# Optimization experiments

Hardware: AMD Instinct MI355X
Metric: run time of the kernel (lower is better)

## Reference

```python
import jax, jax.numpy as jnp
import numpy as np

# dims: B batch, N seq, D model_dim, R lora rank, C codebooks, K codebook_input_channel, P kv pairs, M per-codebook output
B, N, D, R, C, K, P = 4, 2048, 1024, 8, 64, 16, 64
M = (D * R) // C  # 128


def setup_inputs() -> dict:
    key = jax.random.key(0)
    ks = jax.random.split(key, 7)
    x = jax.random.normal(ks[0], (B, N, D), dtype=jnp.float32)
    W_A = jax.random.normal(ks[1], (C, K, D), dtype=jnp.float32) * (D ** -0.5)
    emb_A = jax.random.uniform(ks[2], (C, P, K), dtype=jnp.float32, minval=-1.5, maxval=1.5)
    vals_A = jax.random.normal(ks[3], (C, P, M), dtype=jnp.float32)
    W_B = jax.random.normal(ks[4], (C, K, D), dtype=jnp.float32) * (D ** -0.5)
    emb_B = jax.random.uniform(ks[5], (C, P, K), dtype=jnp.float32, minval=-1.5, maxval=1.5)
    vals_B = jax.random.normal(ks[6], (C, P, M), dtype=jnp.float32)
    return {"x": x, "W_A": W_A, "emb_A": emb_A, "vals_A": vals_A,
            "W_B": W_B, "emb_B": emb_B, "vals_B": vals_B}


def _discrete_kv(x, W, emb, vals):
    # x: [B,N,D]; W: [C,K,D] (Linear weight per codebook); emb: [C,P,K]; vals: [C,P,M]
    proj = jnp.einsum('bnd,ckd->cbnk', x, W)  # per-codebook linear projection
    # squared euclidean distance to each key (argmin is same as cdist argmin)
    d2 = (jnp.sum(proj * proj, axis=-1, keepdims=True)
          - 2.0 * jnp.einsum('cbnk,cpk->cbnp', proj, emb)
          + jnp.sum(emb * emb, axis=-1)[:, None, None, :])  # [C,B,N,P]
    idx = jnp.argmin(d2, axis=-1)                      # [C,B,N]
    y = jax.vmap(lambda v, i: v[i])(vals, idx)          # [C,B,N,M]
    # concat over codebooks on last dim -> [B,N,C*M], then view as [B,N,R,D]
    return jnp.transpose(y, (1, 2, 0, 3)).reshape(x.shape[0], x.shape[1], R, D)


def reference(x, W_A, emb_A, vals_A, W_B, emb_B, vals_B):
    A = _discrete_kv(x, W_A, emb_A, vals_A)   # [B,N,R,D]
    Bm = _discrete_kv(x, W_B, emb_B, vals_B)  # [B,N,R,D]
    t = jnp.einsum('bnd,bnrd->bnr', x, A)
    return jnp.einsum('bnr,bnrd->bnd', t, Bm)
```

## Files before the change

### kernel.cpp

```cpp
#include <hip/hip_runtime.h>

#define NTOK   8192
#define DMODEL 1024
#define NC     64
#define NK     16
#define NP     64
#define NM     128
#define LCAP   (1 << 18)
#define MARGIN 2e-3f

typedef _Float16 f16x8  __attribute__((ext_vector_type(8)));
typedef float    f32x16 __attribute__((ext_vector_type(16)));

#define AS1 __attribute__((address_space(1)))
#define AS3 __attribute__((address_space(3)))

__device__ __forceinline__ void glds16(const void* g, void* l) {
    __builtin_amdgcn_global_load_lds((const AS1 void*)g, (AS3 void*)l, 16, 0, 0);
}

__global__ __launch_bounds__(256) void k_split(
    const float* __restrict__ x, const float* __restrict__ W_A, const float* __restrict__ W_B,
    short* __restrict__ xh, short* __restrict__ xl,
    short* __restrict__ whA, short* __restrict__ wlA,
    short* __restrict__ whB, short* __restrict__ wlB)
{
    const int t = blockIdx.x * 256 + threadIdx.x;
    const int NX = 128 * NTOK;
    const int NW = 128 * 1024;

    const float* src;
    short *dh, *dl;
    if (t < NX) {
        const int chunk = t >> 13, tok = t & 8191;
        src = x + (size_t)tok * DMODEL + chunk * 8;
        dh = xh + (size_t)t * 8;  dl = xl + (size_t)t * 8;
    } else if (t < NX + NW) {
        const int u = t - NX, chunk = u >> 10, ck = u & 1023;
        src = W_A + (size_t)ck * DMODEL + chunk * 8;
        dh = whA + (size_t)u * 8; dl = wlA + (size_t)u * 8;
    } else {
        const int u = t - NX - NW, chunk = u >> 10, ck = u & 1023;
        src = W_B + (size_t)ck * DMODEL + chunk * 8;
        dh = whB + (size_t)u * 8; dl = wlB + (size_t)u * 8;
    }

    const float4 a = *(const float4*)src;
    const float4 b = *(const float4*)(src + 4);
    const float v[8] = {a.x, a.y, a.z, a.w, b.x, b.y, b.z, b.w};
    unsigned h[8], l[8];
    #pragma unroll
    for (int j = 0; j < 8; ++j) {
        const _Float16 hf = (_Float16)v[j];
        const _Float16 lf = (_Float16)(v[j] - (float)hf);
        h[j] = (unsigned)__builtin_bit_cast(unsigned short, hf);
        l[j] = (unsigned)__builtin_bit_cast(unsigned short, lf);
    }
    *(int4*)dh = make_int4((int)(h[0] | (h[1] << 16)), (int)(h[2] | (h[3] << 16)),
                           (int)(h[4] | (h[5] << 16)), (int)(h[6] | (h[7] << 16)));
    *(int4*)dl = make_int4((int)(l[0] | (l[1] << 16)), (int)(l[2] | (l[3] << 16)),
                           (int)(l[4] | (l[5] << 16)), (int)(l[6] | (l[7] << 16)));
}

__global__ __launch_bounds__(512, 1) void k_mfma_argmin(
    const short* __restrict__ xh, const short* __restrict__ xl,
    const short* __restrict__ whA, const short* __restrict__ wlA,
    const short* __restrict__ whB, const short* __restrict__ wlB,
    const float* __restrict__ emb_A, const float* __restrict__ emb_B,
    int* __restrict__ idxbuf, int* __restrict__ list, int* __restrict__ cnt)
{
    __shared__ __align__(16) float smem[32768];
    short* ls = (short*)smem;
    float* projT = smem;
    float* embS  = smem + 16640;
    float* e2S   = smem + 24832;

    const int tid = threadIdx.x;
    const int bid = blockIdx.x;
    const int swz = (bid & 7) * 32 + (bid >> 3);
    const int tb  = swz >> 3;
    const int ot  = swz & 7;
    const int set = ot >> 2;
    const short* __restrict__ wh = set ? whB : whA;
    const short* __restrict__ wl = set ? wlB : wlA;
    const float* __restrict__ Ep = set ? emb_B : emb_A;
    const int ckbase = (ot & 3) * 256;

    const int lane = tid & 63;
    const int wid  = tid >> 6;
    const int wr   = wid >> 2;
    const int wc   = wid & 3;
    const int lr31 = lane & 31;
    const int lk2  = lane >> 5;

    f32x16 acc[4][2];
    #pragma unroll
    for (int m = 0; m < 4; ++m)
        #pragma unroll
        for (int n = 0; n < 2; ++n)
            #pragma unroll
            for (int r = 0; r < 16; ++r) acc[m][n][r] = 0.f;

    const size_t oA0 = ((size_t)(tid >> 8) * NTOK + tb * 256 + (tid & 255)) * 8;
    const size_t oA1 = ((size_t)((tid + 512) >> 8) * NTOK + tb * 256 + (tid & 255)) * 8;
    const size_t oB0 = ((size_t)(tid >> 8) * 1024 + ckbase + (tid & 255)) * 8;
    const size_t oB1 = ((size_t)((tid + 512) >> 8) * 1024 + ckbase + (tid & 255)) * 8;

    #define STAGE(buf, st)                                                   \
        do {                                                                 \
            const size_t sa_ = (size_t)(st) * (4 * NTOK * 8);                \
            const size_t sb_ = (size_t)(st) * (4 * 1024 * 8);                \
            short* lb_ = ls + (buf) * 32768 + tid * 8;                       \
            glds16(xh + oA0 + sa_, lb_);                                     \
            glds16(xh + oA1 + sa_, lb_ + 4096);                              \
            glds16(xl + oA0 + sa_, lb_ + 8192);                              \
            glds16(xl + oA1 + sa_, lb_ + 12288);                             \
            glds16(wh + oB0 + sb_, lb_ + 16384);                             \
            glds16(wh + oB1 + sb_, lb_ + 20480);                             \
            glds16(wl + oB0 + sb_, lb_ + 24576);                             \
            glds16(wl + oB1 + sb_, lb_ + 28672);                             \
        } while (0)

    STAGE(0, 0);
    for (int t = 0; t < 32; ++t) {
        const int cur = t & 1;
        if (t < 31) {
            STAGE(cur ^ 1, t + 1);
            asm volatile("s_waitcnt vmcnt(8)" ::: "memory");
        } else {
            asm volatile("s_waitcnt vmcnt(0)" ::: "memory");
        }
        __builtin_amdgcn_sched_barrier(0);
        __builtin_amdgcn_s_barrier();

        const short* pbuf = ls + cur * 32768;
        #pragma unroll
        for (int ks = 0; ks < 2; ++ks) {
            const int kc2 = ks * 2 + lk2;
            const short* pa = pbuf + (kc2 * 256 + wr * 128 + lr31) * 8;
            const short* pB = pbuf + 16384 + (kc2 * 256 + wc * 64 + lr31) * 8;
            f16x8 ah[4], al[4], bh[2], bl[2];
            #pragma unroll
            for (int m = 0; m < 4; ++m) {
                ah[m] = *(const f16x8*)(pa + m * 256);
                al[m] = *(const f16x8*)(pa + 8192 + m * 256);
            }
            #pragma unroll
            for (int n = 0; n < 2; ++n) {
                bh[n] = *(const f16x8*)(pB + n * 256);
                bl[n] = *(const f16x8*)(pB + 8192 + n * 256);
            }
            #pragma unroll
            for (int m = 0; m < 4; ++m)
                #pragma unroll
                for (int n = 0; n < 2; ++n) {
                    acc[m][n] = __builtin_amdgcn_mfma_f32_32x32x16_f16(ah[m], bh[n], acc[m][n], 0, 0, 0);
                    acc[m][n] = __builtin_amdgcn_mfma_f32_32x32x16_f16(ah[m], bl[n], acc[m][n], 0, 0, 0);
                    acc[m][n] = __builtin_amdgcn_mfma_f32_32x32x16_f16(al[m], bh[n], acc[m][n], 0, 0, 0);
                }
        }
        __builtin_amdgcn_s_barrier();
    }
    #undef STAGE

    #pragma unroll
    for (int ch = 0; ch < 2; ++ch) {
        __syncthreads();
        {
            const float4* eg = (const float4*)(Ep + (size_t)((ot & 3) * 16 + ch * 8) * NP * NK);
            float4* es = (float4*)embS;
            #pragma unroll
            for (int i = 0; i < 4; ++i) es[tid + 512 * i] = eg[tid + 512 * i];
        }
        __syncthreads();
        {
            const float* e = embS + tid * 16;
            float s = 0.f;
            #pragma unroll
            for (int k = 0; k < 16; ++k) s = fmaf(e[k], e[k], s);
            e2S[tid] = s;
        }
        #pragma unroll
        for (int c = 0; c < 4; ++c) {
            __syncthreads();
            if (wr == (c >> 1)) {
                #pragma unroll
                for (int mi = 0; mi < 2; ++mi) {
                    const int m = (c & 1) * 2 + mi;
                    #pragma unroll
                    for (int n = 0; n < 2; ++n) {
                        const int col = wc * 64 + n * 32 + lr31;
                        #pragma unroll
                        for (int r = 0; r < 16; ++r) {
                            const int trow = mi * 32 + (r & 3) + 8 * (r >> 2) + 4 * lk2;
                            projT[col * 65 + trow] = acc[m][n][r];
                        }
                    }
                }
            }
            __syncthreads();
            {
                const int lt = tid & 63, cbl = tid >> 6;
                float pr[16];
                #pragma unroll
                for (int k = 0; k < 16; ++k)
                    pr[k] = projT[((ch * 8 + cbl) * 16 + k) * 65 + lt];
                const float4* eb4 = (const float4*)(embS + cbl * 1024);
                const float* e2 = e2S + cbl * 64;
                float best = 1e30f, second = 1e30f;
                int bp = 0;
                for (int p = 0; p < 64; ++p) {
                    const float4 e0 = eb4[p * 4 + 0], e1 = eb4[p * 4 + 1];
                    const float4 e2v = eb4[p * 4 + 2], e3 = eb4[p * 4 + 3];
                    float s = 0.f;
                    s = fmaf(pr[0], e0.x, s);   s = fmaf(pr[1], e0.y, s);
                    s = fmaf(pr[2], e0.z, s);   s = fmaf(pr[3], e0.w, s);
                    s = fmaf(pr[4], e1.x, s);   s = fmaf(pr[5], e1.y, s);
                    s = fmaf(pr[6], e1.z, s);   s = fmaf(pr[7], e1.w, s);
                    s = fmaf(pr[8], e2v.x, s);  s = fmaf(pr[9], e2v.y, s);
                    s = fmaf(pr[10], e2v.z, s); s = fmaf(pr[11], e2v.w, s);
                    s = fmaf(pr[12], e3.x, s);  s = fmaf(pr[13], e3.y, s);
                    s = fmaf(pr[14], e3.z, s);  s = fmaf(pr[15], e3.w, s);
                    const float g = fmaf(-2.f, s, e2[p]);
                    if (g < best) { second = best; best = g; bp = p; }
                    else if (g < second) { second = g; }
                }
                const int cbook = (ot & 3) * 16 + ch * 8 + cbl;
                const int gtok = tb * 256 + c * 64 + lt;
                idxbuf[(set * NC + cbook) * NTOK + gtok] = bp;
                if (second - best < MARGIN) {
                    const int slot = atomicAdd(cnt, 1);
                    if (slot < LCAP) list[slot] = (set << 19) | (cbook << 13) | gtok;
                }
            }
        }
    }
}

__global__ __launch_bounds__(256) void k_refine(
    const float* __restrict__ x,
    const float* __restrict__ W_A, const float* __restrict__ W_B,
    const float* __restrict__ emb_A, const float* __restrict__ emb_B,
    const int* __restrict__ list, const int* __restrict__ cnt,
    int* __restrict__ idxbuf)
{
    int n = *cnt;
    if (n > LCAP) n = LCAP;
    const int lane = threadIdx.x & 63;
    const int wave = (int)((blockIdx.x * blockDim.x + threadIdx.x) >> 6);
    const int nw   = (int)((gridDim.x * blockDim.x) >> 6);

    for (int i = wave; i < n; i += nw) {
        const int code = list[i];
        const int tok = code & 8191;
        const int c   = (code >> 13) & 63;
        const int set = (code >> 19) & 1;
        const float* __restrict__ Wp = set ? W_B : W_A;
        const float* __restrict__ Ep = set ? emb_B : emb_A;

        double pk[16];
        #pragma unroll
        for (int k = 0; k < 16; ++k) pk[k] = 0.0;
        for (int dd = 0; dd < 16; ++dd) {
            const int d = dd * 64 + lane;
            const double xv = (double)x[(size_t)tok * DMODEL + d];
            #pragma unroll
            for (int k = 0; k < 16; ++k)
                pk[k] = fma(xv, (double)Wp[(size_t)(c * 16 + k) * DMODEL + d], pk[k]);
        }
        #pragma unroll
        for (int k = 0; k < 16; ++k) {
            #pragma unroll
            for (int off = 32; off; off >>= 1)
                pk[k] += __shfl_xor(pk[k], off, 64);
        }
        double d2 = 0.0;
        #pragma unroll
        for (int k = 0; k < 16; ++k) {
            const double t = pk[k] - (double)Ep[(size_t)(c * NP + lane) * NK + k];
            d2 = fma(t, t, d2);
        }
        int bp = lane;
        double bv = d2;
        #pragma unroll
        for (int off = 32; off; off >>= 1) {
            const double ov = __shfl_xor(bv, off, 64);
            const int    op = __shfl_xor(bp, off, 64);
            if (ov < bv || (ov == bv && op < bp)) { bv = ov; bp = op; }
        }
        if (lane == 0) idxbuf[(set * NC + c) * NTOK + tok] = bp;
    }
}

__global__ __launch_bounds__(256) void k_combine(
    const float* __restrict__ x,
    const float* __restrict__ vals_A, const float* __restrict__ vals_B,
    const int* __restrict__ idxbuf, float* __restrict__ out)
{
    __shared__ float xsh[1032];
    __shared__ float part[256];
    __shared__ float tsh[8];
    __shared__ int sIA[64];
    __shared__ int sIB[64];

    const int tid = threadIdx.x;
    const int tok = blockIdx.x;

    if (tid < 64) {
        sIA[tid] = idxbuf[tid * NTOK + tok];
        sIB[tid] = idxbuf[(NC + tid) * NTOK + tok];
    }
    {
        const float4 v = *(const float4*)(x + (size_t)tok * DMODEL + tid * 4);
        const int base = tid * 4 + (tid >> 5);
        xsh[base + 0] = v.x;
        xsh[base + 1] = v.y;
        xsh[base + 2] = v.z;
        xsh[base + 3] = v.w;
    }
    __syncthreads();
    {
        const int c = tid & 63, mseg = tid >> 6;
        const int ia = sIA[c];
        const float4* va = (const float4*)(vals_A + (size_t)(c * NP + ia) * NM + mseg * 32);
        const float* xb = xsh + (c & 7) * 129 + mseg * 32;
        float s = 0.f;
        #pragma unroll
        for (int i = 0; i < 8; ++i) {
            const float4 v = va[i];
            s = fmaf(v.x, xb[i * 4 + 0], s);
            s = fmaf(v.y, xb[i * 4 + 1], s);
            s = fmaf(v.z, xb[i * 4 + 2], s);
            s = fmaf(v.w, xb[i * 4 + 3], s);
        }
        part[tid] = s;
    }
    __syncthreads();
    if (tid < 8) {
        float s = 0.f;
        #pragma unroll
        for (int m = 0; m < 4; ++m)
            #pragma unroll
            for (int j = 0; j < 8; ++j)
                s += part[m * 64 + tid * 8 + j];
        tsh[tid] = s;
    }
    __syncthreads();
    {
        const int d0 = tid * 4, dblk = tid >> 5, dm = d0 & 127;
        float o0 = 0.f, o1 = 0.f, o2 = 0.f, o3 = 0.f;
        #pragma unroll
        for (int r = 0; r < 8; ++r) {
            const int cb = 8 * r + dblk;
            const int ib = sIB[cb];
            const float4 v = *(const float4*)(vals_B + (size_t)(cb * NP + ib) * NM + dm);
            const float tv = tsh[r];
            o0 = fmaf(tv, v.x, o0);
            o1 = fmaf(tv, v.y, o1);
            o2 = fmaf(tv, v.z, o2);
            o3 = fmaf(tv, v.w, o3);
        }
        *(float4*)(out + (size_t)tok * DMODEL + d0) = make_float4(o0, o1, o2, o3);
    }
}

extern "C" void kernel_launch(void* const* d_in, const int* in_sizes, int n_in,
                              void* d_out, int out_size, void* d_ws, size_t ws_size,
                              hipStream_t stream)
{
    const float* x      = (const float*)d_in[0];
    const float* W_A    = (const float*)d_in[1];
    const float* emb_A  = (const float*)d_in[2];
    const float* vals_A = (const float*)d_in[3];
    const float* W_B    = (const float*)d_in[4];
    const float* emb_B  = (const float*)d_in[5];
    const float* vals_B = (const float*)d_in[6];
    float* out = (float*)d_out;

    char* w = (char*)d_ws;
    int*   cnt    = (int*)w;
    int*   list   = (int*)(w + 16);
    int*   idxbuf = (int*)(w + 16 + sizeof(int) * (size_t)LCAP);
    size_t off = 16 + sizeof(int) * (size_t)LCAP + sizeof(int) * (size_t)(2 * NC * NTOK);
    short* xh  = (short*)(w + off); off += (size_t)NTOK * DMODEL * 2;
    short* xl  = (short*)(w + off); off += (size_t)NTOK * DMODEL * 2;
    short* whA = (short*)(w + off); off += (size_t)1024 * DMODEL * 2;
    short* wlA = (short*)(w + off); off += (size_t)1024 * DMODEL * 2;
    short* whB = (short*)(w + off); off += (size_t)1024 * DMODEL * 2;
    short* wlB = (short*)(w + off);

    hipMemsetAsync(cnt, 0, sizeof(int), stream);
    k_split<<<5120, 256, 0, stream>>>(x, W_A, W_B, xh, xl, whA, wlA, whB, wlB);
    k_mfma_argmin<<<256, 512, 0, stream>>>(xh, xl, whA, wlA, whB, wlB,
                                           emb_A, emb_B, idxbuf, list, cnt);
    k_refine<<<1024, 256, 0, stream>>>(x, W_A, W_B, emb_A, emb_B, list, cnt, idxbuf);
    k_combine<<<NTOK, 256, 0, stream>>>(x, vals_A, vals_B, idxbuf, out);
}
```

Baseline: 242.0 us.

## Split GEMM main loop into four phases interleaving prefetch with MFMA bursts

Reorganizes the split-fp16 projection GEMM loop into four barrier-separated phases. Each phase loads a subset of A/B fragments from LDS, issues part of the next stage's global-to-LDS prefetch, and then runs a prioritized MFMA cluster using s_setprio. The intent is to interleave memory issue with matrix work across waves and to reduce register pressure from holding all fragments at once. In exchange it adds more barriers per iteration and moves the vmcnt wait to the end of each iteration, which may expose prefetch latency.

```diff
diff --git a/kernel.cpp b/kernel.cpp
--- a/kernel.cpp
+++ b/kernel.cpp
@@ -102,66 +102,85 @@
             for (int r = 0; r < 16; ++r) acc[m][n][r] = 0.f;
 
     const size_t oA0 = ((size_t)(tid >> 8) * NTOK + tb * 256 + (tid & 255)) * 8;
-    const size_t oA1 = ((size_t)((tid + 512) >> 8) * NTOK + tb * 256 + (tid & 255)) * 8;
+    const size_t oA1 = (((size_t)(tid >> 8) + 2) * NTOK + tb * 256 + (tid & 255)) * 8;
     const size_t oB0 = ((size_t)(tid >> 8) * 1024 + ckbase + (tid & 255)) * 8;
-    const size_t oB1 = ((size_t)((tid + 512) >> 8) * 1024 + ckbase + (tid & 255)) * 8;
-
-    #define STAGE(buf, st)                                                   \
+    const size_t oB1 = (((size_t)(tid >> 8) + 2) * 1024 + ckbase + (tid & 255)) * 8;
+
+    #define STAGE_A(buf, st)                                                 \
         do {                                                                 \
             const size_t sa_ = (size_t)(st) * (4 * NTOK * 8);                \
-            const size_t sb_ = (size_t)(st) * (4 * 1024 * 8);                \
             short* lb_ = ls + (buf) * 32768 + tid * 8;                       \
             glds16(xh + oA0 + sa_, lb_);                                     \
             glds16(xh + oA1 + sa_, lb_ + 4096);                              \
             glds16(xl + oA0 + sa_, lb_ + 8192);                              \
             glds16(xl + oA1 + sa_, lb_ + 12288);                             \
+        } while (0)
+    #define STAGE_B(buf, st)                                                 \
+        do {                                                                 \
+            const size_t sb_ = (size_t)(st) * (4 * 1024 * 8);                \
+            short* lb_ = ls + (buf) * 32768 + tid * 8;                       \
             glds16(wh + oB0 + sb_, lb_ + 16384);                             \
             glds16(wh + oB1 + sb_, lb_ + 20480);                             \
             glds16(wl + oB0 + sb_, lb_ + 24576);                             \
             glds16(wl + oB1 + sb_, lb_ + 28672);                             \
         } while (0)
 
-    STAGE(0, 0);
+    #define TRIPLE(AH, AL, N, M)                                                           \
+        acc[M][N] = __builtin_amdgcn_mfma_f32_32x32x16_f16(AH, vbh##N, acc[M][N], 0, 0, 0); \
+        acc[M][N] = __builtin_amdgcn_mfma_f32_32x32x16_f16(AH, vbl##N, acc[M][N], 0, 0, 0); \
+        acc[M][N] = __builtin_amdgcn_mfma_f32_32x32x16_f16(AL, vbh##N, acc[M][N], 0, 0, 0);
+
+    #define PHASE(KS, MH, DO_B, STAGE_CODE, DO_VM)                                   \
+        do {                                                                         \
+            const short* pbuf_ = ls + cur * 32768;                                   \
+            const int ab_ = (((KS) * 2 + lk2) * 256 + wr * 128 + (MH) * 64 + lr31) * 8; \
+            const f16x8 a0_ = *(const f16x8*)(pbuf_ + ab_);                          \
+            const f16x8 a1_ = *(const f16x8*)(pbuf_ + ab_ + 256);                    \
+            const f16x8 l0_ = *(const f16x8*)(pbuf_ + 8192 + ab_);                   \
+            const f16x8 l1_ = *(const f16x8*)(pbuf_ + 8192 + ab_ + 256);             \
+            if (DO_B) {                                                             \
+                const int bb_ = 16384 + (((KS) * 2 + lk2) * 256 + wc * 64 + lr31) * 8; \
+                vbh0 = *(const f16x8*)(pbuf_ + bb_);                                 \
+                vbh1 = *(const f16x8*)(pbuf_ + bb_ + 256);                           \
+                vbl0 = *(const f16x8*)(pbuf_ + bb_ + 8192);                          \
+                vbl1 = *(const f16x8*)(pbuf_ + bb_ + 8192 + 256);                    \
+            }                                                                        \
+            STAGE_CODE;                                                             \
+            __builtin_amdgcn_s_barrier();                                            \
+            asm volatile("s_waitcnt lgkmcnt(0)" ::: "memory");                       \
+            __builtin_amdgcn_sched_barrier(0);                                       \
+            __builtin_amdgcn_s_setprio(1);                                           \
+            TRIPLE(a0_, l0_, 0, (MH) * 2 + 0)                                        \
+            TRIPLE(a0_, l0_, 1, (MH) * 2 + 0)                                        \
+            TRIPLE(a1_, l1_, 0, (MH) * 2 + 1)                                        \
+            TRIPLE(a1_, l1_, 1, (MH) * 2 + 1)                                        \
+            __builtin_amdgcn_s_setprio(0);                                           \
+            if (DO_VM) {                                                             \
+                asm volatile("s_waitcnt vmcnt(0)" ::: "memory");                     \
+                __builtin_amdgcn_sched_barrier(0);                                   \
+            }                                                                        \
+            __builtin_amdgcn_s_barrier();                                            \
+        } while (0)
+
+    STAGE_A(0, 0);
+    STAGE_B(0, 0);
+    asm volatile("s_waitcnt vmcnt(0)" ::: "memory");
+    __builtin_amdgcn_s_barrier();
+
     for (int t = 0; t < 32; ++t) {
         const int cur = t & 1;
-        if (t < 31) {
-            STAGE(cur ^ 1, t + 1);
-            asm volatile("s_waitcnt vmcnt(8)" ::: "memory");
-        } else {
-            asm volatile("s_waitcnt vmcnt(0)" ::: "memory");
-        }
-        __builtin_amdgcn_sched_barrier(0);
-        __builtin_amdgcn_s_barrier();
-
-        const short* pbuf = ls + cur * 32768;
-        #pragma unroll
-        for (int ks = 0; ks < 2; ++ks) {
-            const int kc2 = ks * 2 + lk2;
-            const short* pa = pbuf + (kc2 * 256 + wr * 128 + lr31) * 8;
-            const short* pB = pbuf + 16384 + (kc2 * 256 + wc * 64 + lr31) * 8;
-            f16x8 ah[4], al[4], bh[2], bl[2];
-            #pragma unroll
-            for (int m = 0; m < 4; ++m) {
-                ah[m] = *(const f16x8*)(pa + m * 256);
-                al[m] = *(const f16x8*)(pa + 8192 + m * 256);
-            }
-            #pragma unroll
-            for (int n = 0; n < 2; ++n) {
-                bh[n] = *(const f16x8*)(pB + n * 256);
-                bl[n] = *(const f16x8*)(pB + 8192 + n * 256);
-            }
-            #pragma unroll
-            for (int m = 0; m < 4; ++m)
-                #pragma unroll
-                for (int n = 0; n < 2; ++n) {
-                    acc[m][n] = __builtin_amdgcn_mfma_f32_32x32x16_f16(ah[m], bh[n], acc[m][n], 0, 0, 0);
-                    acc[m][n] = __builtin_amdgcn_mfma_f32_32x32x16_f16(ah[m], bl[n], acc[m][n], 0, 0, 0);
-                    acc[m][n] = __builtin_amdgcn_mfma_f32_32x32x16_f16(al[m], bh[n], acc[m][n], 0, 0, 0);
-                }
-        }
-        __builtin_amdgcn_s_barrier();
-    }
-    #undef STAGE
+        const int nxt = cur ^ 1;
+        const bool pf = (t < 31);
+        f16x8 vbh0, vbh1, vbl0, vbl1;
+        PHASE(0, 0, true,  { if (pf) STAGE_A(nxt, t + 1); }, false);
+        PHASE(0, 1, false, { if (pf) STAGE_B(nxt, t + 1); }, false);
+        PHASE(1, 0, true,  {}, false);
+        PHASE(1, 1, false, {}, true);
+    }
+    #undef PHASE
+    #undef TRIPLE
+    #undef STAGE_A
+    #undef STAGE_B
 
     #pragma unroll
     for (int ch = 0; ch < 2; ++ch) {
```

Result: no change. 241.6 us (-0.2%).

## Deepen GEMM pipeline to four LDS stages with half-size k-steps

Applied to the files above, without the earlier changes.

The projection GEMM main loop moves from a double-buffered 32-step loop with two k-substeps to a 4-slot ring buffer with 64 smaller steps and three stages of loads in flight. Fragments are read from LDS before the next global-to-LDS copy is issued, which removes the trailing barrier per iteration. The MFMA block is wrapped in raised wave priority. This trades more barriers and loop iterations, plus smaller load batches, for deeper memory latency hiding. The LDS footprint stays the same, but the ring-slot reuse depends on the single barrier per step.

```diff
diff --git a/kernel.cpp b/kernel.cpp
--- a/kernel.cpp
+++ b/kernel.cpp
@@ -101,67 +101,66 @@
             #pragma unroll
             for (int r = 0; r < 16; ++r) acc[m][n][r] = 0.f;
 
-    const size_t oA0 = ((size_t)(tid >> 8) * NTOK + tb * 256 + (tid & 255)) * 8;
-    const size_t oA1 = ((size_t)((tid + 512) >> 8) * NTOK + tb * 256 + (tid & 255)) * 8;
-    const size_t oB0 = ((size_t)(tid >> 8) * 1024 + ckbase + (tid & 255)) * 8;
-    const size_t oB1 = ((size_t)((tid + 512) >> 8) * 1024 + ckbase + (tid & 255)) * 8;
+    const size_t oA = ((size_t)(tid >> 8) * NTOK + tb * 256 + (tid & 255)) * 8;
+    const size_t oB = ((size_t)(tid >> 8) * 1024 + ckbase + (tid & 255)) * 8;
 
     #define STAGE(buf, st)                                                   \
         do {                                                                 \
-            const size_t sa_ = (size_t)(st) * (4 * NTOK * 8);                \
-            const size_t sb_ = (size_t)(st) * (4 * 1024 * 8);                \
-            short* lb_ = ls + (buf) * 32768 + tid * 8;                       \
-            glds16(xh + oA0 + sa_, lb_);                                     \
-            glds16(xh + oA1 + sa_, lb_ + 4096);                              \
-            glds16(xl + oA0 + sa_, lb_ + 8192);                              \
-            glds16(xl + oA1 + sa_, lb_ + 12288);                             \
-            glds16(wh + oB0 + sb_, lb_ + 16384);                             \
-            glds16(wh + oB1 + sb_, lb_ + 20480);                             \
-            glds16(wl + oB0 + sb_, lb_ + 24576);                             \
-            glds16(wl + oB1 + sb_, lb_ + 28672);                             \
+            const size_t sa_ = (size_t)(st) * (size_t)(2 * NTOK * 8);        \
+            const size_t sb_ = (size_t)(st) * (size_t)(2 * 1024 * 8);        \
+            short* lb_ = ls + (buf) * 16384 + tid * 8;                       \
+            glds16(xh + oA + sa_, lb_);                                      \
+            glds16(xl + oA + sa_, lb_ + 4096);                               \
+            glds16(wh + oB + sb_, lb_ + 8192);                               \
+            glds16(wl + oB + sb_, lb_ + 12288);                              \
         } while (0)
 
+    const int aoff = (lk2 * 256 + wr * 128 + lr31) * 8;
+    const int boff = 8192 + (lk2 * 256 + wc * 64 + lr31) * 8;
+
     STAGE(0, 0);
-    for (int t = 0; t < 32; ++t) {
-        const int cur = t & 1;
-        if (t < 31) {
-            STAGE(cur ^ 1, t + 1);
-            asm volatile("s_waitcnt vmcnt(8)" ::: "memory");
-        } else {
-            asm volatile("s_waitcnt vmcnt(0)" ::: "memory");
-        }
+    STAGE(1, 1);
+    STAGE(2, 2);
+
+    for (int t = 0; t < 64; ++t) {
+        asm volatile("s_waitcnt vmcnt(8)" ::: "memory");
+        __builtin_amdgcn_s_barrier();
+
+        const short* bb = ls + (t & 3) * 16384;
+        f16x8 ah[4], al[4], bh[2], bl[2];
+        #pragma unroll
+        for (int m = 0; m < 4; ++m) {
+            ah[m] = *(const f16x8*)(bb + aoff + m * 256);
+            al[m] = *(const f16x8*)(bb + 4096 + aoff + m * 256);
+        }
+        #pragma unroll
+        for (int n = 0; n < 2; ++n) {
+            bh[n] = *(const f16x8*)(bb + boff + n * 256);
+            bl[n] = *(const f16x8*)(bb + 8192 - 8192 + 12288 - 12288 + 4096 + boff + n * 256);
+        }
+
+        {
+            const int ts = (t + 3 < 64) ? (t + 3) : 63;
+            STAGE((t + 3) & 3, ts);
+        }
+
+        asm volatile("s_waitcnt lgkmcnt(0)" ::: "memory");
         __builtin_amdgcn_sched_barrier(0);
-        __builtin_amdgcn_s_barrier();
-
-        const short* pbuf = ls + cur * 32768;
-        #pragma unroll
-        for (int ks = 0; ks < 2; ++ks) {
-            const int kc2 = ks * 2 + lk2;
-            const short* pa = pbuf + (kc2 * 256 + wr * 128 + lr31) * 8;
-            const short* pB = pbuf + 16384 + (kc2 * 256 + wc * 64 + lr31) * 8;
-            f16x8 ah[4], al[4], bh[2], bl[2];
-            #pragma unroll
-            for (int m = 0; m < 4; ++m) {
-                ah[m] = *(const f16x8*)(pa + m * 256);
-                al[m] = *(const f16x8*)(pa + 8192 + m * 256);
+        __builtin_amdgcn_s_setprio(1);
+        #pragma unroll
+        for (int m = 0; m < 4; ++m)
+            #pragma unroll
+            for (int n = 0; n < 2; ++n) {
+                acc[m][n] = __builtin_amdgcn_mfma_f32_32x32x16_f16(ah[m], bh[n], acc[m][n], 0, 0, 0);
+                acc[m][n] = __builtin_amdgcn_mfma_f32_32x32x16_f16(ah[m], bl[n], acc[m][n], 0, 0, 0);
+                acc[m][n] = __builtin_amdgcn_mfma_f32_32x32x16_f16(al[m], bh[n], acc[m][n], 0, 0, 0);
             }
-            #pragma unroll
-            for (int n = 0; n < 2; ++n) {
-                bh[n] = *(const f16x8*)(pB + n * 256);
-                bl[n] = *(const f16x8*)(pB + 8192 + n * 256);
-            }
-            #pragma unroll
-            for (int m = 0; m < 4; ++m)
-                #pragma unroll
-                for (int n = 0; n < 2; ++n) {
-                    acc[m][n] = __builtin_amdgcn_mfma_f32_32x32x16_f16(ah[m], bh[n], acc[m][n], 0, 0, 0);
-                    acc[m][n] = __builtin_amdgcn_mfma_f32_32x32x16_f16(ah[m], bl[n], acc[m][n], 0, 0, 0);
-                    acc[m][n] = __builtin_amdgcn_mfma_f32_32x32x16_f16(al[m], bh[n], acc[m][n], 0, 0, 0);
-                }
-        }
-        __builtin_amdgcn_s_barrier();
+        __builtin_amdgcn_s_setprio(0);
     }
     #undef STAGE
+
+    asm volatile("s_waitcnt vmcnt(0)" ::: "memory");
+    __builtin_amdgcn_s_barrier();
 
     #pragma unroll
     for (int ch = 0; ch < 2; ++ch) {
```

New measurement: 242.4 us. About the same (+0.2%).
